# Optimization experiments

Measured on AMD Instinct MI355X. Metric: run time of the kernel, lower is better.

The kernel has to match this reference:

```python
import jax, jax.numpy as jnp
import numpy as np

N_HEADS = 16
D_EMBED = 1024
D_HEAD = D_EMBED // N_HEADS
B, S = 2, 2048


def setup_inputs() -> dict:
    key = jax.random.key(0)
    ks = jax.random.split(key, 5)
    scale = 1.0 / np.sqrt(D_EMBED)
    return {
        "x": jax.random.normal(ks[0], (B, S, D_EMBED), dtype=jnp.float32),
        "w_qkv": jax.random.normal(ks[1], (D_EMBED, 3 * D_EMBED), dtype=jnp.float32) * scale,
        "b_qkv": jax.random.normal(ks[2], (3 * D_EMBED,), dtype=jnp.float32) * 0.01,
        "w_out": jax.random.normal(ks[3], (D_EMBED, D_EMBED), dtype=jnp.float32) * scale,
        "b_out": jax.random.normal(ks[4], (D_EMBED,), dtype=jnp.float32) * 0.01,
    }


def reference(x, w_qkv, b_qkv, w_out, b_out):
    b, s, d = x.shape
    # fused QKV projection, then split into q, k, v each [b, s, d]
    qkv = x @ w_qkv + b_qkv
    q, k, v = jnp.split(qkv, 3, axis=-1)
    # reshape to [b, heads, s, d_head]
    def heads(t):
        return t.reshape(b, s, N_HEADS, D_HEAD).transpose(0, 2, 1, 3)
    q, k, v = heads(q), heads(k), heads(v)
    # scaled dot-product attention (no causal mask, dropout off / eval mode)
    scores = jnp.einsum("bhqd,bhkd->bhqk", q, k) / jnp.sqrt(jnp.float32(D_HEAD))
    weights = jax.nn.softmax(scores, axis=-1)
    out = jnp.einsum("bhqk,bhkd->bhqd", weights, v)
    out = out.transpose(0, 2, 1, 3).reshape(b, s, d)
    return out @ w_out + b_out
```

## Files before the change

### kernel.cpp

```cpp
#include <hip/hip_runtime.h>
#include <hip/hip_bf16.h>
#include <cstdint>
#include <cstddef>

#define NHEADS 16
#define DHEAD  64
#define BATCH  2
#define SEQ    2048
#define DEMB   1024
#define TOK    (BATCH*SEQ)
#define NQKV   (3*DEMB)

typedef __bf16 bf16;
typedef __bf16 bf16x8 __attribute__((ext_vector_type(8)));
typedef __bf16 bf16x4 __attribute__((ext_vector_type(4)));
typedef float  f32x4  __attribute__((ext_vector_type(4)));

static __device__ __forceinline__ void gload_lds16(const bf16* g, bf16* l) {
    __builtin_amdgcn_global_load_lds(
        (const __attribute__((address_space(1))) unsigned*)g,
        (__attribute__((address_space(3))) unsigned*)l, 16, 0, 0);
}

__global__ __launch_bounds__(256) void cvt_bf16(const float* __restrict__ in,
                                                bf16* __restrict__ out, int n) {
    int i = (blockIdx.x * blockDim.x + threadIdx.x) * 4;
    if (i + 3 < n) {
        float4 v = *(const float4*)&in[i];
        bf16x4 o;
        o[0] = (bf16)v.x; o[1] = (bf16)v.y; o[2] = (bf16)v.z; o[3] = (bf16)v.w;
        *(bf16x4*)&out[i] = o;
    }
}

__global__ __launch_bounds__(256) void transpose_cvt(const float* __restrict__ in,
                                                     bf16* __restrict__ out,
                                                     int R, int C) {
    __shared__ float t[32][33];
    int c0 = blockIdx.x * 32, r0 = blockIdx.y * 32;
    int tx = threadIdx.x & 31, ty = threadIdx.x >> 5;
    #pragma unroll
    for (int i = 0; i < 32; i += 8)
        t[ty + i][tx] = in[(size_t)(r0 + ty + i) * C + c0 + tx];
    __syncthreads();
    #pragma unroll
    for (int i = 0; i < 32; i += 8)
        out[(size_t)(c0 + ty + i) * R + r0 + tx] = (bf16)t[tx][ty + i];
}

#define BM 128
#define BN 128
#define BK 32

__global__ __launch_bounds__(256)
void gemm_bias(const bf16* __restrict__ A, const bf16* __restrict__ Bt,
               const float* __restrict__ bias, int mode,
               bf16* __restrict__ Qb, bf16* __restrict__ Kb,
               bf16* __restrict__ Vt, float* __restrict__ Cout) {
    __shared__ __align__(16) bf16 As[2][BM * BK];
    __shared__ __align__(16) bf16 Bs[2][BN * BK];
    const int K = 1024;
    const int tid = threadIdx.x;
    const int lane = tid & 63, wid = tid >> 6;
    const int gm0 = blockIdx.y * BM, gn0 = blockIdx.x * BN;
    const int wm = (wid >> 1) * 64, wn = (wid & 1) * 64;

    f32x4 acc[4][4];
    #pragma unroll
    for (int i = 0; i < 4; i++)
        #pragma unroll
        for (int j = 0; j < 4; j++)
            #pragma unroll
            for (int e = 0; e < 4; e++) acc[i][j][e] = 0.f;

    int a_off[4], b_off[4];
    #pragma unroll
    for (int f = 0; f < 4; f++) {
        int ra = wm + f * 16 + (lane & 15);
        a_off[f] = ra * BK + (((lane >> 4) ^ ((ra >> 1) & 3)) << 3);
        int rb = wn + f * 16 + (lane & 15);
        b_off[f] = rb * BK + (((lane >> 4) ^ ((rb >> 1) & 3)) << 3);
    }
    int srow[2], scol[2];
    #pragma unroll
    for (int i = 0; i < 2; i++) {
        int o = tid * 16 + i * 4096;
        int r = o >> 6;
        int c = (o >> 4) & 3;
        srow[i] = r;
        scol[i] = ((c ^ ((r >> 1) & 3)) << 3);
    }

    const int NKT = K / BK;
    int cur = 0;
    #pragma unroll
    for (int i = 0; i < 2; i++) {
        gload_lds16(&A[(size_t)(gm0 + srow[i]) * K + scol[i]],  &As[0][wid * 512 + i * 2048]);
        gload_lds16(&Bt[(size_t)(gn0 + srow[i]) * K + scol[i]], &Bs[0][wid * 512 + i * 2048]);
    }
    __syncthreads();
    for (int kt = 0; kt < NKT; ++kt) {
        if (kt + 1 < NKT) {
            int k0 = (kt + 1) * BK;
            #pragma unroll
            for (int i = 0; i < 2; i++) {
                gload_lds16(&A[(size_t)(gm0 + srow[i]) * K + k0 + scol[i]],
                            &As[cur ^ 1][wid * 512 + i * 2048]);
                gload_lds16(&Bt[(size_t)(gn0 + srow[i]) * K + k0 + scol[i]],
                            &Bs[cur ^ 1][wid * 512 + i * 2048]);
            }
        }
        bf16x8 af[4], bfr[4];
        #pragma unroll
        for (int f = 0; f < 4; f++) af[f]  = *(const bf16x8*)&As[cur][a_off[f]];
        #pragma unroll
        for (int f = 0; f < 4; f++) bfr[f] = *(const bf16x8*)&Bs[cur][b_off[f]];
        #pragma unroll
        for (int i = 0; i < 4; i++)
            #pragma unroll
            for (int j = 0; j < 4; j++)
                acc[i][j] = __builtin_amdgcn_mfma_f32_16x16x32_bf16(af[i], bfr[j], acc[i][j], 0, 0, 0);
        __syncthreads();
        cur ^= 1;
    }

    const int col_base = gn0 + wn + (lane & 15);
    const int row_base = gm0 + wm + ((lane >> 4) << 2);
    if (mode == 0) {
        #pragma unroll
        for (int j = 0; j < 4; j++) {
            int col = col_base + j * 16;
            float bv = bias[col];
            int sec = col >> 10;
            int within = col & 1023;
            int h = within >> 6, d = within & 63;
            #pragma unroll
            for (int i = 0; i < 4; i++)
                #pragma unroll
                for (int r = 0; r < 4; r++) {
                    int tok = row_base + i * 16 + r;
                    int b = tok >> 11, s = tok & 2047;
                    int bh = b * NHEADS + h;
                    bf16 v = (bf16)(acc[i][j][r] + bv);
                    if (sec == 0)      Qb[((size_t)bh * SEQ + s) * DHEAD + d] = v;
                    else if (sec == 1) Kb[((size_t)bh * SEQ + s) * DHEAD + d] = v;
                    else               Vt[((size_t)bh * DHEAD + d) * SEQ + s] = v;
                }
        }
    } else {
        #pragma unroll
        for (int j = 0; j < 4; j++) {
            int col = col_base + j * 16;
            float bv = bias[col];
            #pragma unroll
            for (int i = 0; i < 4; i++)
                #pragma unroll
                for (int r = 0; r < 4; r++) {
                    int tok = row_base + i * 16 + r;
                    Cout[(size_t)tok * DEMB + col] = acc[i][j][r] + bv;
                }
        }
    }
}

__global__ __launch_bounds__(256)
void attn_fwd(const bf16* __restrict__ Qb, const bf16* __restrict__ Kb,
              const bf16* __restrict__ Vt, bf16* __restrict__ attn_out) {
    __shared__ __align__(16) bf16 Pl[4][32 * 64];
    const int tid = threadIdx.x, lane = tid & 63, wid = tid >> 6;
    const int bid = blockIdx.x;
    const int bh = (bid & 7) * 4 + ((bid >> 3) >> 4);
    const int q0 = ((bid >> 3) & 15) * 128 + wid * 32;
    const bf16* Qh = Qb + (size_t)bh * SEQ * DHEAD;
    const bf16* Kh = Kb + (size_t)bh * SEQ * DHEAD;
    const bf16* Vh = Vt + (size_t)bh * DHEAD * SEQ;
    bf16* Pw = &Pl[wid][0];

    bf16x8 qf[2][2];
    #pragma unroll
    for (int mf = 0; mf < 2; mf++)
        #pragma unroll
        for (int kf = 0; kf < 2; kf++)
            qf[mf][kf] = *(const bf16x8*)&Qh[(size_t)(q0 + mf * 16 + (lane & 15)) * DHEAD
                                            + kf * 32 + ((lane >> 4) << 3)];

    f32x4 oacc[2][4];
    #pragma unroll
    for (int i = 0; i < 2; i++)
        #pragma unroll
        for (int j = 0; j < 4; j++)
            #pragma unroll
            for (int e = 0; e < 4; e++) oacc[i][j][e] = 0.f;
    float mrun[2][4], lrun[2][4];
    #pragma unroll
    for (int i = 0; i < 2; i++)
        #pragma unroll
        for (int r = 0; r < 4; r++) { mrun[i][r] = -INFINITY; lrun[i][r] = 0.f; }

    const float SC = 0.125f * 1.44269504088896f;

    for (int kv0 = 0; kv0 < SEQ; kv0 += 64) {
        f32x4 sacc[2][4];
        #pragma unroll
        for (int i = 0; i < 2; i++)
            #pragma unroll
            for (int j = 0; j < 4; j++)
                #pragma unroll
                for (int e = 0; e < 4; e++) sacc[i][j][e] = 0.f;
        #pragma unroll
        for (int kf = 0; kf < 2; kf++) {
            bf16x8 kfr[4];
            #pragma unroll
            for (int nf = 0; nf < 4; nf++)
                kfr[nf] = *(const bf16x8*)&Kh[(size_t)(kv0 + nf * 16 + (lane & 15)) * DHEAD
                                              + kf * 32 + ((lane >> 4) << 3)];
            __builtin_amdgcn_s_setprio(1);
            #pragma unroll
            for (int mf = 0; mf < 2; mf++)
                #pragma unroll
                for (int nf = 0; nf < 4; nf++)
                    sacc[mf][nf] = __builtin_amdgcn_mfma_f32_16x16x32_bf16(qf[mf][kf], kfr[nf], sacc[mf][nf], 0, 0, 0);
            __builtin_amdgcn_s_setprio(0);
        }
        #pragma unroll
        for (int mf = 0; mf < 2; mf++)
            #pragma unroll
            for (int r = 0; r < 4; r++) {
                float s0 = sacc[mf][0][r] * SC, s1 = sacc[mf][1][r] * SC;
                float s2 = sacc[mf][2][r] * SC, s3 = sacc[mf][3][r] * SC;
                float mx = fmaxf(fmaxf(s0, s1), fmaxf(s2, s3));
                mx = fmaxf(mx, __shfl_xor(mx, 1));
                mx = fmaxf(mx, __shfl_xor(mx, 2));
                mx = fmaxf(mx, __shfl_xor(mx, 4));
                mx = fmaxf(mx, __shfl_xor(mx, 8));
                float mnew = fmaxf(mrun[mf][r], mx);
                float corr = exp2f(mrun[mf][r] - mnew);
                float p0 = exp2f(s0 - mnew), p1 = exp2f(s1 - mnew);
                float p2 = exp2f(s2 - mnew), p3 = exp2f(s3 - mnew);
                float ps = p0 + p1 + p2 + p3;
                ps += __shfl_xor(ps, 1);
                ps += __shfl_xor(ps, 2);
                ps += __shfl_xor(ps, 4);
                ps += __shfl_xor(ps, 8);
                lrun[mf][r] = lrun[mf][r] * corr + ps;
                mrun[mf][r] = mnew;
                #pragma unroll
                for (int nf = 0; nf < 4; nf++) oacc[mf][nf][r] *= corr;
                sacc[mf][0][r] = p0; sacc[mf][1][r] = p1;
                sacc[mf][2][r] = p2; sacc[mf][3][r] = p3;
            }
        #pragma unroll
        for (int mf = 0; mf < 2; mf++)
            #pragma unroll
            for (int nf = 0; nf < 4; nf++)
                #pragma unroll
                for (int r = 0; r < 4; r++) {
                    int row = mf * 16 + ((lane >> 4) << 2) + r;
                    int col = nf * 16 + (lane & 15);
                    int addr = row * 64 + (((col >> 3) ^ (row & 7)) << 3) + (col & 7);
                    Pw[addr] = (bf16)sacc[mf][nf][r];
                }
        #pragma unroll
        for (int kf = 0; kf < 2; kf++) {
            bf16x8 pf[2], vf[4];
            #pragma unroll
            for (int mf = 0; mf < 2; mf++) {
                int row = mf * 16 + (lane & 15);
                int cc = kf * 4 + (lane >> 4);
                pf[mf] = *(const bf16x8*)&Pw[row * 64 + ((cc ^ (row & 7)) << 3)];
            }
            #pragma unroll
            for (int nf = 0; nf < 4; nf++)
                vf[nf] = *(const bf16x8*)&Vh[(size_t)(nf * 16 + (lane & 15)) * SEQ
                                             + kv0 + kf * 32 + ((lane >> 4) << 3)];
            __builtin_amdgcn_s_setprio(1);
            #pragma unroll
            for (int mf = 0; mf < 2; mf++)
                #pragma unroll
                for (int nf = 0; nf < 4; nf++)
                    oacc[mf][nf] = __builtin_amdgcn_mfma_f32_16x16x32_bf16(pf[mf], vf[nf], oacc[mf][nf], 0, 0, 0);
            __builtin_amdgcn_s_setprio(0);
        }
    }
    const int b = bh >> 4, h = bh & 15;
    #pragma unroll
    for (int mf = 0; mf < 2; mf++) {
        float inv[4];
        #pragma unroll
        for (int r = 0; r < 4; r++) inv[r] = 1.0f / lrun[mf][r];
        #pragma unroll
        for (int nf = 0; nf < 4; nf++)
            #pragma unroll
            for (int r = 0; r < 4; r++) {
                int s = q0 + mf * 16 + ((lane >> 4) << 2) + r;
                int d = nf * 16 + (lane & 15);
                attn_out[((size_t)b * SEQ + s) * DEMB + h * DHEAD + d] =
                    (bf16)(oacc[mf][nf][r] * inv[r]);
            }
    }
}

extern "C" void kernel_launch(void* const* d_in, const int* in_sizes, int n_in,
                              void* d_out, int out_size, void* d_ws, size_t ws_size,
                              hipStream_t stream) {
    const float* x     = (const float*)d_in[0];
    const float* w_qkv = (const float*)d_in[1];
    const float* b_qkv = (const float*)d_in[2];
    const float* w_out = (const float*)d_in[3];
    const float* b_out = (const float*)d_in[4];
    float* out = (float*)d_out;

    bf16* xb    = (bf16*)d_ws;
    bf16* wqkvT = xb    + (size_t)TOK * DEMB;
    bf16* woutT = wqkvT + (size_t)NQKV * DEMB;
    bf16* Qb    = woutT + (size_t)DEMB * DEMB;
    bf16* Kb    = Qb    + (size_t)BATCH * NHEADS * SEQ * DHEAD;
    bf16* Vt    = Kb    + (size_t)BATCH * NHEADS * SEQ * DHEAD;
    bf16* attnO = xb;

    cvt_bf16<<<(TOK * DEMB) / (256 * 4), 256, 0, stream>>>(x, xb, TOK * DEMB);
    transpose_cvt<<<dim3(NQKV / 32, DEMB / 32), 256, 0, stream>>>(w_qkv, wqkvT, DEMB, NQKV);
    transpose_cvt<<<dim3(DEMB / 32, DEMB / 32), 256, 0, stream>>>(w_out, woutT, DEMB, DEMB);
    gemm_bias<<<dim3(NQKV / BN, TOK / BM), 256, 0, stream>>>(xb, wqkvT, b_qkv, 0,
                                                             Qb, Kb, Vt, nullptr);
    attn_fwd<<<BATCH * NHEADS * (SEQ / 128), 256, 0, stream>>>(Qb, Kb, Vt, attnO);
    gemm_bias<<<dim3(DEMB / BN, TOK / BM), 256, 0, stream>>>(attnO, woutT, b_out, 1,
                                                             nullptr, nullptr, nullptr, out);
}
```

Measured before the change: 313.2 us.

## Transpose score MFMA, prescale Q, and defer softmax max rescaling

The QKV GEMM epilogue now folds the softmax scale and log2(e) into Q, which removes the per-score multiply in attention. The S=K·Q^T MFMA operands are swapped so each lane holds one query's scores across its registers. Row max and sum then need only two cross-lane shuffles instead of four per row, and P is written to LDS as packed bf16x4 stores. A lazy-rescale rule skips the exp2 correction and the O rescale while the new max exceeds the running max by no more than 8, which saves work but lets unnormalized values grow by up to 2^8.

```diff
diff --git a/kernel.cpp b/kernel.cpp
--- a/kernel.cpp
+++ b/kernel.cpp
@@ -51,6 +51,7 @@
 #define BM 128
 #define BN 128
 #define BK 32
+#define QSC 0.180336880138855f
 
 __global__ __launch_bounds__(256)
 void gemm_bias(const bf16* __restrict__ A, const bf16* __restrict__ Bt,
@@ -141,10 +142,10 @@
                     int tok = row_base + i * 16 + r;
                     int b = tok >> 11, s = tok & 2047;
                     int bh = b * NHEADS + h;
-                    bf16 v = (bf16)(acc[i][j][r] + bv);
-                    if (sec == 0)      Qb[((size_t)bh * SEQ + s) * DHEAD + d] = v;
-                    else if (sec == 1) Kb[((size_t)bh * SEQ + s) * DHEAD + d] = v;
-                    else               Vt[((size_t)bh * DHEAD + d) * SEQ + s] = v;
+                    float fv = acc[i][j][r] + bv;
+                    if (sec == 0)      Qb[((size_t)bh * SEQ + s) * DHEAD + d] = (bf16)(fv * QSC);
+                    else if (sec == 1) Kb[((size_t)bh * SEQ + s) * DHEAD + d] = (bf16)fv;
+                    else               Vt[((size_t)bh * DHEAD + d) * SEQ + s] = (bf16)fv;
                 }
         }
     } else {
@@ -168,6 +169,7 @@
               const bf16* __restrict__ Vt, bf16* __restrict__ attn_out) {
     __shared__ __align__(16) bf16 Pl[4][32 * 64];
     const int tid = threadIdx.x, lane = tid & 63, wid = tid >> 6;
+    const int g = lane >> 4;
     const int bid = blockIdx.x;
     const int bh = (bid & 7) * 4 + ((bid >> 3) >> 4);
     const int q0 = ((bid >> 3) & 15) * 128 + wid * 32;
@@ -182,7 +184,7 @@
         #pragma unroll
         for (int kf = 0; kf < 2; kf++)
             qf[mf][kf] = *(const bf16x8*)&Qh[(size_t)(q0 + mf * 16 + (lane & 15)) * DHEAD
-                                            + kf * 32 + ((lane >> 4) << 3)];
+                                            + kf * 32 + (g << 3)];
 
     f32x4 oacc[2][4];
     #pragma unroll
@@ -191,13 +193,8 @@
         for (int j = 0; j < 4; j++)
             #pragma unroll
             for (int e = 0; e < 4; e++) oacc[i][j][e] = 0.f;
-    float mrun[2][4], lrun[2][4];
-    #pragma unroll
-    for (int i = 0; i < 2; i++)
-        #pragma unroll
-        for (int r = 0; r < 4; r++) { mrun[i][r] = -INFINITY; lrun[i][r] = 0.f; }
-
-    const float SC = 0.125f * 1.44269504088896f;
+    float mrun[2] = {-INFINITY, -INFINITY};
+    float lrun[2] = {0.f, 0.f};
 
     for (int kv0 = 0; kv0 < SEQ; kv0 += 64) {
         f32x4 sacc[2][4];
@@ -213,66 +210,87 @@
             #pragma unroll
             for (int nf = 0; nf < 4; nf++)
                 kfr[nf] = *(const bf16x8*)&Kh[(size_t)(kv0 + nf * 16 + (lane & 15)) * DHEAD
-                                              + kf * 32 + ((lane >> 4) << 3)];
+                                              + kf * 32 + (g << 3)];
             __builtin_amdgcn_s_setprio(1);
             #pragma unroll
             for (int mf = 0; mf < 2; mf++)
                 #pragma unroll
                 for (int nf = 0; nf < 4; nf++)
-                    sacc[mf][nf] = __builtin_amdgcn_mfma_f32_16x16x32_bf16(qf[mf][kf], kfr[nf], sacc[mf][nf], 0, 0, 0);
+                    sacc[mf][nf] = __builtin_amdgcn_mfma_f32_16x16x32_bf16(kfr[nf], qf[mf][kf], sacc[mf][nf], 0, 0, 0);
             __builtin_amdgcn_s_setprio(0);
         }
+
+        float mx[2];
+        #pragma unroll
+        for (int mf = 0; mf < 2; mf++) {
+            float a = fmaxf(fmaxf(sacc[mf][0][0], sacc[mf][0][1]),
+                            fmaxf(sacc[mf][0][2], sacc[mf][0][3]));
+            float b = fmaxf(fmaxf(sacc[mf][1][0], sacc[mf][1][1]),
+                            fmaxf(sacc[mf][1][2], sacc[mf][1][3]));
+            float c = fmaxf(fmaxf(sacc[mf][2][0], sacc[mf][2][1]),
+                            fmaxf(sacc[mf][2][2], sacc[mf][2][3]));
+            float d = fmaxf(fmaxf(sacc[mf][3][0], sacc[mf][3][1]),
+                            fmaxf(sacc[mf][3][2], sacc[mf][3][3]));
+            float m = fmaxf(fmaxf(a, b), fmaxf(c, d));
+            m = fmaxf(m, __shfl_xor(m, 16));
+            m = fmaxf(m, __shfl_xor(m, 32));
+            mx[mf] = m;
+        }
+        const bool defer = __all(fmaxf(mx[0] - mrun[0], mx[1] - mrun[1]) <= 8.0f);
+        #pragma unroll
+        for (int mf = 0; mf < 2; mf++) {
+            float mnew = defer ? mrun[mf] : fmaxf(mrun[mf], mx[mf]);
+            float corr = 1.0f;
+            if (!defer) {
+                corr = exp2f(mrun[mf] - mnew);
+                #pragma unroll
+                for (int rr = 0; rr < 4; rr++) {
+                    float c = __shfl(corr, (g << 2) + rr);
+                    #pragma unroll
+                    for (int nf = 0; nf < 4; nf++) oacc[mf][nf][rr] *= c;
+                }
+                mrun[mf] = mnew;
+            }
+            float psum = 0.f;
+            #pragma unroll
+            for (int nf = 0; nf < 4; nf++)
+                #pragma unroll
+                for (int rr = 0; rr < 4; rr++) {
+                    float p = exp2f(sacc[mf][nf][rr] - mnew);
+                    sacc[mf][nf][rr] = p;
+                    psum += p;
+                }
+            psum += __shfl_xor(psum, 16);
+            psum += __shfl_xor(psum, 32);
+            lrun[mf] = lrun[mf] * corr + psum;
+        }
+
         #pragma unroll
         for (int mf = 0; mf < 2; mf++)
             #pragma unroll
-            for (int r = 0; r < 4; r++) {
-                float s0 = sacc[mf][0][r] * SC, s1 = sacc[mf][1][r] * SC;
-                float s2 = sacc[mf][2][r] * SC, s3 = sacc[mf][3][r] * SC;
-                float mx = fmaxf(fmaxf(s0, s1), fmaxf(s2, s3));
-                mx = fmaxf(mx, __shfl_xor(mx, 1));
-                mx = fmaxf(mx, __shfl_xor(mx, 2));
-                mx = fmaxf(mx, __shfl_xor(mx, 4));
-                mx = fmaxf(mx, __shfl_xor(mx, 8));
-                float mnew = fmaxf(mrun[mf][r], mx);
-                float corr = exp2f(mrun[mf][r] - mnew);
-                float p0 = exp2f(s0 - mnew), p1 = exp2f(s1 - mnew);
-                float p2 = exp2f(s2 - mnew), p3 = exp2f(s3 - mnew);
-                float ps = p0 + p1 + p2 + p3;
-                ps += __shfl_xor(ps, 1);
-                ps += __shfl_xor(ps, 2);
-                ps += __shfl_xor(ps, 4);
-                ps += __shfl_xor(ps, 8);
-                lrun[mf][r] = lrun[mf][r] * corr + ps;
-                mrun[mf][r] = mnew;
-                #pragma unroll
-                for (int nf = 0; nf < 4; nf++) oacc[mf][nf][r] *= corr;
-                sacc[mf][0][r] = p0; sacc[mf][1][r] = p1;
-                sacc[mf][2][r] = p2; sacc[mf][3][r] = p3;
-            }
-        #pragma unroll
-        for (int mf = 0; mf < 2; mf++)
-            #pragma unroll
-            for (int nf = 0; nf < 4; nf++)
-                #pragma unroll
-                for (int r = 0; r < 4; r++) {
-                    int row = mf * 16 + ((lane >> 4) << 2) + r;
-                    int col = nf * 16 + (lane & 15);
-                    int addr = row * 64 + (((col >> 3) ^ (row & 7)) << 3) + (col & 7);
-                    Pw[addr] = (bf16)sacc[mf][nf][r];
-                }
+            for (int nf = 0; nf < 4; nf++) {
+                bf16x4 pk;
+                #pragma unroll
+                for (int rr = 0; rr < 4; rr++) pk[rr] = (bf16)sacc[mf][nf][rr];
+                int q = mf * 16 + (lane & 15);
+                int chunk = nf * 2 + (g >> 1);
+                int addr = q * 64 + ((chunk ^ (q & 7)) << 3) + ((g & 1) << 2);
+                *(bf16x4*)&Pw[addr] = pk;
+            }
+
         #pragma unroll
         for (int kf = 0; kf < 2; kf++) {
             bf16x8 pf[2], vf[4];
             #pragma unroll
             for (int mf = 0; mf < 2; mf++) {
                 int row = mf * 16 + (lane & 15);
-                int cc = kf * 4 + (lane >> 4);
+                int cc = kf * 4 + g;
                 pf[mf] = *(const bf16x8*)&Pw[row * 64 + ((cc ^ (row & 7)) << 3)];
             }
             #pragma unroll
             for (int nf = 0; nf < 4; nf++)
                 vf[nf] = *(const bf16x8*)&Vh[(size_t)(nf * 16 + (lane & 15)) * SEQ
-                                             + kv0 + kf * 32 + ((lane >> 4) << 3)];
+                                             + kv0 + kf * 32 + (g << 3)];
             __builtin_amdgcn_s_setprio(1);
             #pragma unroll
             for (int mf = 0; mf < 2; mf++)
@@ -285,17 +303,18 @@
     const int b = bh >> 4, h = bh & 15;
     #pragma unroll
     for (int mf = 0; mf < 2; mf++) {
-        float inv[4];
-        #pragma unroll
-        for (int r = 0; r < 4; r++) inv[r] = 1.0f / lrun[mf][r];
+        float linv = 1.0f / lrun[mf];
+        float linvr[4];
+        #pragma unroll
+        for (int rr = 0; rr < 4; rr++) linvr[rr] = __shfl(linv, (g << 2) + rr);
         #pragma unroll
         for (int nf = 0; nf < 4; nf++)
             #pragma unroll
-            for (int r = 0; r < 4; r++) {
-                int s = q0 + mf * 16 + ((lane >> 4) << 2) + r;
+            for (int rr = 0; rr < 4; rr++) {
+                int s = q0 + mf * 16 + (g << 2) + rr;
                 int d = nf * 16 + (lane & 15);
                 attn_out[((size_t)b * SEQ + s) * DEMB + h * DHEAD + d] =
-                    (bf16)(oacc[mf][nf][r] * inv[r]);
+                    (bf16)(oacc[mf][nf][rr] * linvr[rr]);
             }
     }
 }
```

Result: faster. 295.3 us (-5.7%).
